# Kernel tuning notes

Measured on AMD Instinct MI355X. Metric: run time of the kernel, lower is better.

## Reference

```python
import jax, jax.numpy as jnp
import numpy as np

B, D, H, W = 2, 16, 16, 16
N = D * H * W
CDESC = 64
TEMP = 0.07
TOPK = 24
RADIUS = 0.45


def flatten_spatial(x):
    # (B, C, D, H, W) -> (B, N, C)
    b, c = x.shape[:2]
    return x.reshape(b, c, -1).transpose(0, 2, 1)


def voxel_grid():
    # normalized voxel-center grid in [-1, 1], shape (3, D, H, W)
    zs = jnp.linspace(-1.0, 1.0, D)
    ys = jnp.linspace(-1.0, 1.0, H)
    xs = jnp.linspace(-1.0, 1.0, W)
    return jnp.stack(jnp.meshgrid(zs, ys, xs, indexing='ij'), axis=0)


def setup_inputs() -> dict:
    key = jax.random.key(0)
    ks = jax.random.split(key, 8)
    return {
        'src_canonical': jax.random.normal(ks[0], (B, 3, D, H, W), jnp.float32),
        'tgt_canonical': jax.random.normal(ks[1], (B, 3, D, H, W), jnp.float32),
        'src_desc': jax.random.normal(ks[2], (B, CDESC, D, H, W), jnp.float32),
        'tgt_desc': jax.random.normal(ks[3], (B, CDESC, D, H, W), jnp.float32),
        'src_mlogits': jax.random.normal(ks[4], (B, 2, D, H, W), jnp.float32),
        'tgt_mlogits': jax.random.normal(ks[5], (B, 2, D, H, W), jnp.float32),
        'src_unc': jax.random.uniform(ks[6], (B, 1, D, H, W), jnp.float32),
        'tgt_unc': jax.random.uniform(ks[7], (B, 1, D, H, W), jnp.float32),
    }


def reference(src_canonical, tgt_canonical, src_desc, tgt_desc,
              src_mlogits, tgt_mlogits, src_unc, tgt_unc):
    sc = flatten_spatial(src_canonical)  # (B, N, 3)
    tc = flatten_spatial(tgt_canonical)  # (B, N, 3)
    sd = flatten_spatial(src_desc)       # (B, N, C)
    td = flatten_spatial(tgt_desc)       # (B, N, C)

    # torch.cdist: Euclidean distance matrix (B, N, N)
    d2 = (jnp.sum(sc * sc, -1)[:, :, None]
          + jnp.sum(tc * tc, -1)[:, None, :]
          - 2.0 * jnp.einsum('bid,bjd->bij', sc, tc))
    dist = jnp.sqrt(jnp.maximum(d2, 1e-12))

    sim = jnp.einsum('bid,bjd->bij', sd, td)  # (B, N, N)

    k = min(TOPK, N)
    _, nn_idx = jax.lax.top_k(-dist, k)  # k smallest distances per row
    bidx = jnp.arange(B)[:, None, None]
    ridx = jnp.arange(N)[None, :, None]
    allowed = jnp.zeros((B, N, N), bool).at[bidx, ridx, nn_idx].set(True)
    allowed = allowed | (dist <= RADIUS)

    tgt_match = jax.nn.softmax(flatten_spatial(tgt_mlogits), axis=-1)[..., 0]  # (B, N)
    src_match = jax.nn.softmax(flatten_spatial(src_mlogits), axis=-1)[..., 0]  # (B, N)

    # (B, N, 1) + (B, 1, N) rank-1 uncertainty penalty
    unc = flatten_spatial(src_unc) + flatten_spatial(tgt_unc).transpose(0, 2, 1)

    scores = sim - dist - 0.1 * unc
    scores = jnp.where(allowed, scores, -10000.0)
    # legacy matchability score mode
    scores = scores + jnp.maximum(jnp.log(tgt_match), -20.0)[:, None, :]
    probs = jax.nn.softmax(scores / TEMP, axis=-1)
    probs = jnp.nan_to_num(probs, nan=0.0, posinf=0.0, neginf=0.0)

    tpos = voxel_grid().reshape(3, -1).T  # (N, 3)
    expected = jnp.einsum('bij,jd->bid', probs, tpos)  # (B, N, 3)
    src_pos = jnp.broadcast_to(tpos, (B, N, 3))

    disp = (expected - src_pos).transpose(0, 2, 1).reshape(B, 3, D, H, W)
    disp = jnp.nan_to_num(disp, nan=0.0, posinf=0.0, neginf=0.0)

    conf = (jnp.max(probs, axis=-1) * src_match).reshape(B, 1, D, H, W)

    ent = -jnp.sum(probs * jnp.log(jnp.clip(probs, 1e-12, None)), axis=-1)
    ent = jnp.nan_to_num(ent, nan=0.0, posinf=0.0, neginf=0.0).reshape(B, 1, D, H, W)

    return expected, disp, probs, conf, ent, src_pos
```

## Files before the change

### kernel.cpp

```cpp
#include <hip/hip_runtime.h>
#include <math.h>
#include <stddef.h>

#define NN    4096
#define BATCH 2
#define CD    64
#define KSEL  24
#define RAD2  0.2025f
#define NBINS 256
#define KBASE 1888
#define LCAP  255
#define CCAP  64

typedef float f4v __attribute__((ext_vector_type(4)));

__device__ __forceinline__ int d2key(unsigned bits) {
  int k = (int)(bits >> 19) - KBASE;
  return k < 0 ? 0 : (k > NBINS - 1 ? NBINS - 1 : k);
}

__device__ __forceinline__ int wave_bin24(const int* h0, const int* h1, int lane, int* cb_out) {
  int4 a = ((const int4*)h0)[lane];
  int4 b = ((const int4*)h1)[lane];
  int tt[4] = {a.x + b.x, a.y + b.y, a.z + b.z, a.w + b.w};
  int s = tt[0] + tt[1] + tt[2] + tt[3];
  int inc = s;
#pragma unroll
  for (int off = 1; off < 64; off <<= 1) {
    int t = __shfl_up(inc, off);
    if (lane >= off) inc += t;
  }
  int below = inc - s;
  int Bl = -1, Bb = 0;
#pragma unroll
  for (int q = 0; q < 4; ++q) {
    if (Bl < 0 && below < KSEL && below + tt[q] >= KSEL) { Bl = 4 * lane + q; Bb = below; }
    below += tt[q];
  }
  unsigned long long mk = __ballot(Bl >= 0);
  if (!mk) return -1;
  int sl = __ffsll((long long)mk) - 1;
  *cb_out = __shfl(Bb, sl);
  return __shfl(Bl, sl);
}

__global__ __launch_bounds__(256)
void prep_all(const float* __restrict__ td, const float* __restrict__ sd,
              const float* __restrict__ tml, const float* __restrict__ tu,
              float* __restrict__ tdT, float* __restrict__ sdT,
              float* __restrict__ addj) {
  __shared__ float tile[64][65];
  int blk = blockIdx.x;
  if (blk < 256) {
    const float* src = (blk < 128) ? td  : sd;
    float*       dst = (blk < 128) ? tdT : sdT;
    int lb = blk & 127;
    int b  = lb >> 6;
    int j0 = (lb & 63) << 6;
    int jl = threadIdx.x & 63;
    int cq = threadIdx.x >> 6;
    const float* srcp = src + (size_t)b * CD * NN;
#pragma unroll
    for (int r = 0; r < 16; ++r) {
      int c = r * 4 + cq;
      tile[c][jl] = srcp[(size_t)c * NN + j0 + jl];
    }
    __syncthreads();
    float* dstp = dst + (size_t)b * NN * CD;
#pragma unroll
    for (int r = 0; r < 16; ++r) {
      int j = r * 4 + cq;
      dstp[(size_t)(j0 + j) * CD + jl] = tile[jl][j];
    }
  } else {
    int idx = (blk - 256) * 256 + threadIdx.x;
    if (idx < BATCH * NN) {
      int b = idx >> 12, j = idx & (NN - 1);
      float l0 = tml[(size_t)b * 2 * NN + j];
      float l1 = tml[(size_t)b * 2 * NN + NN + j];
      float x  = l1 - l0;
      float sp = fmaxf(x, 0.0f) + log1pf(expf(-fabsf(x)));
      addj[idx] = fmaxf(-sp, -20.0f) - 0.1f * tu[idx];
    }
  }
}

__global__ __launch_bounds__(256, 8)
void matcher_main(const float* __restrict__ sc, const float* __restrict__ tc,
                  const float* __restrict__ sd, const float* __restrict__ td,
                  const float* __restrict__ tdT, const float* __restrict__ sdT,
                  const float* __restrict__ addj,
                  const float* __restrict__ tml, const float* __restrict__ tu,
                  const float* __restrict__ sml,
                  float* __restrict__ oexp, float* __restrict__ odisp,
                  float* __restrict__ oprob, float* __restrict__ oconf,
                  float* __restrict__ oent, float* __restrict__ osrc) {
  __shared__ __align__(16) unsigned idxb[NN / 4];
  __shared__ __align__(16) int      hist[2][NBINS];
  __shared__ __align__(16) float4   sdp4[CD / 4];
  __shared__ int2     lst[LCAP];
  __shared__ int2     slist[256];
  __shared__ unsigned cand[CCAP];
  __shared__ int      lcount, candn;

  const int tid  = threadIdx.x;
  const int w    = tid >> 6;
  const int lane = tid & 63;
  const int row  = blockIdx.x;
  const int b    = row >> 12;
  const int i    = row & (NN - 1);
  const unsigned RADB = __float_as_uint(RAD2);

  if (tid < 128) ((int4*)hist)[tid] = make_int4(0, 0, 0, 0);
#pragma unroll
  for (int q = 0; q < 4; ++q) idxb[(q << 8) + tid] = 0u;
  if (sdT) { if (tid < 16) sdp4[tid] = ((const float4*)(sdT + ((size_t)b * NN + i) * CD))[tid]; }
  else     { if (tid < 64) ((float*)sdp4)[tid] = sd[(size_t)b * CD * NN + (size_t)tid * NN + i]; }
  if (tid == 0) { lcount = 0; candn = 0; }

  const float* scb = sc + (size_t)b * 3 * NN;
  const float s0 = scb[i], s1 = scb[NN + i], s2 = scb[2 * NN + i];
  const float4* tcx = (const float4*)(tc + (size_t)b * 3 * NN);
  const float4* tcy = tcx + NN / 4;
  const float4* tcz = tcy + NN / 4;
  const int cp = w >> 1;
  __syncthreads();

  unsigned d2b[16];
#pragma unroll
  for (int k = 0; k < 4; ++k) {
    int g = (k << 8) + tid;
    float4 X = tcx[g], Y = tcy[g], Z = tcz[g];
    float xs[4] = {X.x, X.y, X.z, X.w};
    float ys[4] = {Y.x, Y.y, Y.z, Y.w};
    float zs[4] = {Z.x, Z.y, Z.z, Z.w};
#pragma unroll
    for (int r = 0; r < 4; ++r) {
      float dx = xs[r] - s0, dy = ys[r] - s1, dz = zs[r] - s2;
      float d2 = fmaxf(__fmaf_rn(dx, dx, __fmaf_rn(dy, dy, dz * dz)), 1e-12f);
      unsigned bits = __float_as_uint(d2);
      d2b[(k << 2) + r] = bits;
      if (d2 < 2.0f) atomicAdd(&hist[cp][d2key(bits)], 1);
    }
  }
  __syncthreads();

  int cb = 0;
  int Bs = wave_bin24(hist[0], hist[1], lane, &cb);
  if (Bs < 0) {
    __syncthreads();
#pragma unroll
    for (int m = 0; m < 16; ++m)
      if (__uint_as_float(d2b[m]) >= 2.0f) atomicAdd(&hist[cp][d2key(d2b[m])], 1);
    __syncthreads();
    Bs = wave_bin24(hist[0], hist[1], lane, &cb);
  }

#pragma unroll
  for (int m = 0; m < 16; ++m) {
    unsigned bits = d2b[m];
    int key = d2key(bits);
    if (key <= Bs || bits <= RADB) {
      int idx = atomicAdd(&lcount, 1);
      if (idx < LCAP) {
        int j = ((m >> 2) << 10) + (tid << 2) + (m & 3);
        ((unsigned char*)idxb)[j] = (unsigned char)(idx + 1);
        lst[idx] = make_int2(j, (int)bits);
      }
      if (key == Bs) {
        int c = atomicAdd(&candn, 1);
        if (c < CCAP) cand[c] = bits;
      }
    }
  }
  __syncthreads();
  const int na = lcount < LCAP ? lcount : LCAP;

  unsigned thrb;
  {
    int found = 0; unsigned fv = 0;
    const int Krem = KSEL - cb;
    if (candn <= CCAP) {
      int nc = candn;
      if (lane < nc) {
        unsigned v = cand[lane];
        int lt = 0, le = 0;
        for (int m = 0; m < nc; ++m) { unsigned u = cand[m]; lt += (u < v); le += (u <= v); }
        if (lt < Krem && le >= Krem) { found = 1; fv = v; }
      }
    } else {
      for (int e = lane; e < na; e += 64) {
        unsigned v = (unsigned)lst[e].y;
        int lt = 0, le = 0;
        for (int m = 0; m < na; ++m) {
          unsigned u = (unsigned)lst[m].y;
          lt += (u < v); le += (u <= v);
        }
        if (lt < KSEL && le >= KSEL) { found = 1; fv = v; }
      }
    }
    unsigned long long mk = __ballot(found != 0);
    unsigned d24 = (unsigned)__shfl((int)fv, __ffsll((long long)mk) - 1);
    thrb = d24 > RADB ? d24 : RADB;
  }

  const float* tdb = tdT ? tdT + (size_t)b * NN * CD : nullptr;
  if (tid < na) {
    int2 en = lst[tid];
    int j = en.x;
    unsigned bits = (unsigned)en.y;
    float d2 = __uint_as_float(bits);
    float a0 = 0.f, a1 = 0.f, a2 = 0.f, a3 = 0.f;
    if (tdb) {
      const float4* trow = (const float4*)(tdb + (size_t)j * CD);
#pragma unroll
      for (int q = 0; q < CD / 4; q += 4) {
        float4 x0 = sdp4[q],     t0 = trow[q];
        float4 x1 = sdp4[q + 1], t1 = trow[q + 1];
        float4 x2 = sdp4[q + 2], t2 = trow[q + 2];
        float4 x3 = sdp4[q + 3], t3 = trow[q + 3];
        a0 = fmaf(x0.x, t0.x, fmaf(x0.y, t0.y, fmaf(x0.z, t0.z, fmaf(x0.w, t0.w, a0))));
        a1 = fmaf(x1.x, t1.x, fmaf(x1.y, t1.y, fmaf(x1.z, t1.z, fmaf(x1.w, t1.w, a1))));
        a2 = fmaf(x2.x, t2.x, fmaf(x2.y, t2.y, fmaf(x2.z, t2.z, fmaf(x2.w, t2.w, a2))));
        a3 = fmaf(x3.x, t3.x, fmaf(x3.y, t3.y, fmaf(x3.z, t3.z, fmaf(x3.w, t3.w, a3))));
      }
    } else {
      const float* spx = (const float*)sdp4;
      const float* tp  = td + (size_t)b * CD * NN + j;
#pragma unroll 8
      for (int c2 = 0; c2 < CD; ++c2) a0 = fmaf(spx[c2], tp[(size_t)c2 * NN], a0);
    }
    float sim = (a0 + a1) + (a2 + a3);
    float aj;
    if (addj) {
      aj = addj[(size_t)b * NN + j];
    } else {
      float l0 = tml[(size_t)b * 2 * NN + j];
      float l1 = tml[(size_t)b * 2 * NN + NN + j];
      float x  = l1 - l0;
      float sp = fmaxf(x, 0.0f) + log1pf(expf(-fabsf(x)));
      aj = fmaxf(-sp, -20.0f) - 0.1f * tu[(size_t)b * NN + j];
    }
    float sco = (bits <= thrb) ? (sim - sqrtf(d2) + aj) : -1e30f;
    slist[tid] = make_int2(j, __float_as_int(sco));
  }
  __syncthreads();

  const float C1   = (1.0f / 0.07f) * 1.44269504089f;
  const float STEP = 2.0f / 15.0f;
  const float LN2  = 0.69314718056f;
  float m_ = -1e30f;
  for (int e = lane; e < na; e += 64) m_ = fmaxf(m_, __int_as_float(slist[e].y));
#pragma unroll
  for (int off = 32; off; off >>= 1) m_ = fmaxf(m_, __shfl_xor(m_, off));
  float zl = 0.f, eu = 0.f, e0 = 0.f, e1 = 0.f, e2 = 0.f;
  for (int e = lane; e < na; e += 64) {
    int2 sv = slist[e];
    float u  = (__int_as_float(sv.y) - m_) * C1;
    float ev = exp2f(u);
    int j = sv.x;
    float pz = -1.0f + STEP * (float)(j >> 8);
    float py = -1.0f + STEP * (float)((j >> 4) & 15);
    float px = -1.0f + STEP * (float)(j & 15);
    zl += ev; eu = fmaf(ev, u, eu);
    e0 = fmaf(ev, pz, e0); e1 = fmaf(ev, py, e1); e2 = fmaf(ev, px, e2);
  }
#pragma unroll
  for (int off = 32; off; off >>= 1) {
    zl += __shfl_xor(zl, off); eu += __shfl_xor(eu, off);
    e0 += __shfl_xor(e0, off); e1 += __shfl_xor(e1, off); e2 += __shfl_xor(e2, off);
  }
  const float invZ = 1.0f / zl;

  f4v* prow4 = (f4v*)(oprob + (size_t)row * NN);
#pragma unroll
  for (int q = 0; q < 4; ++q) {
    int c = (q << 8) + tid;
    unsigned pk = idxb[c];
    f4v v; v[0] = 0.f; v[1] = 0.f; v[2] = 0.f; v[3] = 0.f;
    if (pk) {
#pragma unroll
      for (int r = 0; r < 4; ++r) {
        unsigned u8 = (pk >> (8 * r)) & 0xFFu;
        if (u8) v[r] = exp2f((__int_as_float(slist[u8 - 1].y) - m_) * C1) * invZ;
      }
    }
    __builtin_nontemporal_store(v, &prow4[c]);
  }

  if (tid == 0) {
    float p0 = e0 * invZ, p1 = e1 * invZ, p2 = e2 * invZ;
    float ent = LN2 * (log2f(zl) - eu * invZ);
    float tz = -1.0f + STEP * (float)(i >> 8);
    float ty = -1.0f + STEP * (float)((i >> 4) & 15);
    float tx = -1.0f + STEP * (float)(i & 15);
    size_t r3 = (size_t)row * 3;
    oexp[r3 + 0] = p0; oexp[r3 + 1] = p1; oexp[r3 + 2] = p2;
    osrc[r3 + 0] = tz; osrc[r3 + 1] = ty; osrc[r3 + 2] = tx;
    size_t db = (size_t)b * 3 * NN;
    odisp[db + 0 * NN + i] = p0 - tz;
    odisp[db + 1 * NN + i] = p1 - ty;
    odisp[db + 2 * NN + i] = p2 - tx;
    float ls0 = sml[(size_t)b * 2 * NN + i];
    float ls1 = sml[(size_t)b * 2 * NN + NN + i];
    float smv = 1.0f / (1.0f + expf(ls1 - ls0));
    oconf[(size_t)b * NN + i] = invZ * smv;
    oent[(size_t)b * NN + i]  = ent;
  }
}

extern "C" void kernel_launch(void* const* d_in, const int* in_sizes, int n_in,
                              void* d_out, int out_size, void* d_ws, size_t ws_size,
                              hipStream_t stream) {
  const float* sc  = (const float*)d_in[0];
  const float* tc  = (const float*)d_in[1];
  const float* sd  = (const float*)d_in[2];
  const float* td  = (const float*)d_in[3];
  const float* sml = (const float*)d_in[4];
  const float* tml = (const float*)d_in[5];
  const float* tu  = (const float*)d_in[7];

  float* out   = (float*)d_out;
  float* oexp  = out;
  float* odisp = oexp  + (size_t)BATCH * NN * 3;
  float* oprob = odisp + (size_t)BATCH * NN * 3;
  float* oconf = oprob + (size_t)BATCH * NN * NN;
  float* oent  = oconf + (size_t)BATCH * NN;
  float* osrc  = oent  + (size_t)BATCH * NN;

  size_t need = ((size_t)2 * BATCH * NN * CD + (size_t)BATCH * NN) * sizeof(float);
  float* tdT = nullptr; float* sdT = nullptr; float* adj = nullptr;
  if (ws_size >= need) {
    tdT = (float*)d_ws;
    sdT = tdT + (size_t)BATCH * NN * CD;
    adj = sdT + (size_t)BATCH * NN * CD;
    prep_all<<<256 + 32, 256, 0, stream>>>(td, sd, tml, tu, tdT, sdT, adj);
  }
  matcher_main<<<BATCH * NN, 256, 0, stream>>>(sc, tc, sd, td, tdT, sdT, adj,
                                               tml, tu, sml,
                                               oexp, odisp, oprob, oconf, oent, osrc);
}
```

Measured before the change: 194.1 us.

## Process two source rows per 512-thread block sharing target coordinate loads

Each block of 512 threads now handles two adjacent source rows. Every target coordinate load is reused for both rows' distance and histogram computation, and the histogram is split into four copies per row to cut atomic contention. Later stages (threshold search, similarity, softmax, prob row store) are split by thread half. This halves the block count and target-coordinate traffic per row, at the cost of more shared memory per block and a heavier launch-bounds target that could lower occupancy or spill registers.

```diff
diff --git a/kernel.cpp b/kernel.cpp
--- a/kernel.cpp
+++ b/kernel.cpp
@@ -11,6 +11,7 @@
 #define KBASE 1888
 #define LCAP  255
 #define CCAP  64
+#define NCP   4
 
 typedef float f4v __attribute__((ext_vector_type(4)));
 
@@ -19,10 +20,13 @@
   return k < 0 ? 0 : (k > NBINS - 1 ? NBINS - 1 : k);
 }
 
-__device__ __forceinline__ int wave_bin24(const int* h0, const int* h1, int lane, int* cb_out) {
-  int4 a = ((const int4*)h0)[lane];
-  int4 b = ((const int4*)h1)[lane];
-  int tt[4] = {a.x + b.x, a.y + b.y, a.z + b.z, a.w + b.w};
+__device__ __forceinline__ int wave_bin24(const int (*h)[NBINS], int lane, int* cb_out) {
+  int4 a = ((const int4*)h[0])[lane];
+  int4 b = ((const int4*)h[1])[lane];
+  int4 c = ((const int4*)h[2])[lane];
+  int4 d = ((const int4*)h[3])[lane];
+  int tt[4] = {a.x + b.x + c.x + d.x, a.y + b.y + c.y + d.y,
+               a.z + b.z + c.z + d.z, a.w + b.w + c.w + d.w};
   int s = tt[0] + tt[1] + tt[2] + tt[3];
   int inc = s;
 #pragma unroll
@@ -85,7 +89,7 @@
   }
 }
 
-__global__ __launch_bounds__(256, 8)
+__global__ __launch_bounds__(512, 8)
 void matcher_main(const float* __restrict__ sc, const float* __restrict__ tc,
                   const float* __restrict__ sd, const float* __restrict__ td,
                   const float* __restrict__ tdT, const float* __restrict__ sdT,
@@ -95,105 +99,133 @@
                   float* __restrict__ oexp, float* __restrict__ odisp,
                   float* __restrict__ oprob, float* __restrict__ oconf,
                   float* __restrict__ oent, float* __restrict__ osrc) {
-  __shared__ __align__(16) unsigned idxb[NN / 4];
-  __shared__ __align__(16) int      hist[2][NBINS];
-  __shared__ __align__(16) float4   sdp4[CD / 4];
-  __shared__ int2     lst[LCAP];
-  __shared__ int2     slist[256];
-  __shared__ unsigned cand[CCAP];
-  __shared__ int      lcount, candn;
+  __shared__ __align__(16) unsigned idxb[2][NN / 4];
+  __shared__ __align__(16) int      hist[2][NCP][NBINS];
+  __shared__ __align__(16) float4   sdp4[2][CD / 4];
+  __shared__ int2     lst[2][LCAP];
+  __shared__ int2     slist[2][256];
+  __shared__ unsigned cand[2][CCAP];
+  __shared__ int      lcount[2], candn[2];
 
   const int tid  = threadIdx.x;
   const int w    = tid >> 6;
   const int lane = tid & 63;
-  const int row  = blockIdx.x;
-  const int b    = row >> 12;
-  const int i    = row & (NN - 1);
+  const int rg   = tid >> 8;
+  const int row0 = blockIdx.x * 2;
+  const int b    = row0 >> 12;
+  const int i0   = row0 & (NN - 1);
   const unsigned RADB = __float_as_uint(RAD2);
 
-  if (tid < 128) ((int4*)hist)[tid] = make_int4(0, 0, 0, 0);
-#pragma unroll
-  for (int q = 0; q < 4; ++q) idxb[(q << 8) + tid] = 0u;
-  if (sdT) { if (tid < 16) sdp4[tid] = ((const float4*)(sdT + ((size_t)b * NN + i) * CD))[tid]; }
-  else     { if (tid < 64) ((float*)sdp4)[tid] = sd[(size_t)b * CD * NN + (size_t)tid * NN + i]; }
-  if (tid == 0) { lcount = 0; candn = 0; }
-
+  ((int4*)hist)[tid] = make_int4(0, 0, 0, 0);
+  ((int4*)idxb)[tid] = make_int4(0, 0, 0, 0);
+  if (tid < 2) { lcount[tid] = 0; candn[tid] = 0; }
+  if (sdT) {
+    if (tid < 32) {
+      int r = tid >> 4, t = tid & 15;
+      sdp4[r][t] = ((const float4*)(sdT + ((size_t)b * NN + i0 + r) * CD))[t];
+    }
+  } else if (tid < 128) {
+    int r = tid >> 6, c = tid & 63;
+    ((float*)sdp4[r])[c] = sd[(size_t)b * CD * NN + (size_t)c * NN + i0 + r];
+  }
   const float* scb = sc + (size_t)b * 3 * NN;
-  const float s0 = scb[i], s1 = scb[NN + i], s2 = scb[2 * NN + i];
+  const float sA0 = scb[i0],     sA1 = scb[NN + i0],     sA2 = scb[2 * NN + i0];
+  const float sB0 = scb[i0 + 1], sB1 = scb[NN + i0 + 1], sB2 = scb[2 * NN + i0 + 1];
   const float4* tcx = (const float4*)(tc + (size_t)b * 3 * NN);
   const float4* tcy = tcx + NN / 4;
   const float4* tcz = tcy + NN / 4;
-  const int cp = w >> 1;
+  const int cp = w & (NCP - 1);
   __syncthreads();
 
-  unsigned d2b[16];
-#pragma unroll
-  for (int k = 0; k < 4; ++k) {
-    int g = (k << 8) + tid;
+  unsigned dA[8], dB[8];
+#pragma unroll
+  for (int k = 0; k < 2; ++k) {
+    int g = (k << 9) + tid;
     float4 X = tcx[g], Y = tcy[g], Z = tcz[g];
     float xs[4] = {X.x, X.y, X.z, X.w};
     float ys[4] = {Y.x, Y.y, Y.z, Y.w};
     float zs[4] = {Z.x, Z.y, Z.z, Z.w};
 #pragma unroll
     for (int r = 0; r < 4; ++r) {
-      float dx = xs[r] - s0, dy = ys[r] - s1, dz = zs[r] - s2;
+      float dx = xs[r] - sA0, dy = ys[r] - sA1, dz = zs[r] - sA2;
       float d2 = fmaxf(__fmaf_rn(dx, dx, __fmaf_rn(dy, dy, dz * dz)), 1e-12f);
       unsigned bits = __float_as_uint(d2);
-      d2b[(k << 2) + r] = bits;
-      if (d2 < 2.0f) atomicAdd(&hist[cp][d2key(bits)], 1);
+      dA[(k << 2) + r] = bits;
+      if (d2 < 2.0f) atomicAdd(&hist[0][cp][d2key(bits)], 1);
+      dx = xs[r] - sB0; dy = ys[r] - sB1; dz = zs[r] - sB2;
+      d2 = fmaxf(__fmaf_rn(dx, dx, __fmaf_rn(dy, dy, dz * dz)), 1e-12f);
+      bits = __float_as_uint(d2);
+      dB[(k << 2) + r] = bits;
+      if (d2 < 2.0f) atomicAdd(&hist[1][cp][d2key(bits)], 1);
     }
   }
   __syncthreads();
 
-  int cb = 0;
-  int Bs = wave_bin24(hist[0], hist[1], lane, &cb);
-  if (Bs < 0) {
+  int cbA = 0, cbB = 0;
+  int BsA = wave_bin24(hist[0], lane, &cbA);
+  int BsB = wave_bin24(hist[1], lane, &cbB);
+  if (BsA < 0 || BsB < 0) {
     __syncthreads();
-#pragma unroll
-    for (int m = 0; m < 16; ++m)
-      if (__uint_as_float(d2b[m]) >= 2.0f) atomicAdd(&hist[cp][d2key(d2b[m])], 1);
+    if (BsA < 0) {
+#pragma unroll
+      for (int m = 0; m < 8; ++m)
+        if (__uint_as_float(dA[m]) >= 2.0f) atomicAdd(&hist[0][cp][d2key(dA[m])], 1);
+    }
+    if (BsB < 0) {
+#pragma unroll
+      for (int m = 0; m < 8; ++m)
+        if (__uint_as_float(dB[m]) >= 2.0f) atomicAdd(&hist[1][cp][d2key(dB[m])], 1);
+    }
     __syncthreads();
-    Bs = wave_bin24(hist[0], hist[1], lane, &cb);
-  }
-
-#pragma unroll
-  for (int m = 0; m < 16; ++m) {
-    unsigned bits = d2b[m];
+    if (BsA < 0) BsA = wave_bin24(hist[0], lane, &cbA);
+    if (BsB < 0) BsB = wave_bin24(hist[1], lane, &cbB);
+  }
+
+#pragma unroll
+  for (int m = 0; m < 8; ++m) {
+    int j = ((m >> 2) << 11) + (tid << 2) + (m & 3);
+    unsigned bits = dA[m];
     int key = d2key(bits);
-    if (key <= Bs || bits <= RADB) {
-      int idx = atomicAdd(&lcount, 1);
+    if (key <= BsA || bits <= RADB) {
+      int idx = atomicAdd(&lcount[0], 1);
       if (idx < LCAP) {
-        int j = ((m >> 2) << 10) + (tid << 2) + (m & 3);
-        ((unsigned char*)idxb)[j] = (unsigned char)(idx + 1);
-        lst[idx] = make_int2(j, (int)bits);
-      }
-      if (key == Bs) {
-        int c = atomicAdd(&candn, 1);
-        if (c < CCAP) cand[c] = bits;
-      }
+        ((unsigned char*)idxb[0])[j] = (unsigned char)(idx + 1);
+        lst[0][idx] = make_int2(j, (int)bits);
+      }
+      if (key == BsA) { int cc = atomicAdd(&candn[0], 1); if (cc < CCAP) cand[0][cc] = bits; }
+    }
+    bits = dB[m];
+    key = d2key(bits);
+    if (key <= BsB || bits <= RADB) {
+      int idx = atomicAdd(&lcount[1], 1);
+      if (idx < LCAP) {
+        ((unsigned char*)idxb[1])[j] = (unsigned char)(idx + 1);
+        lst[1][idx] = make_int2(j, (int)bits);
+      }
+      if (key == BsB) { int cc = atomicAdd(&candn[1], 1); if (cc < CCAP) cand[1][cc] = bits; }
     }
   }
   __syncthreads();
-  const int na = lcount < LCAP ? lcount : LCAP;
+  const int nag = (lcount[rg] < LCAP) ? lcount[rg] : LCAP;
 
   unsigned thrb;
   {
     int found = 0; unsigned fv = 0;
-    const int Krem = KSEL - cb;
-    if (candn <= CCAP) {
-      int nc = candn;
-      if (lane < nc) {
-        unsigned v = cand[lane];
+    const int Krem = KSEL - (rg ? cbB : cbA);
+    const int ncg  = candn[rg];
+    if (ncg <= CCAP) {
+      if (lane < ncg) {
+        unsigned v = cand[rg][lane];
         int lt = 0, le = 0;
-        for (int m = 0; m < nc; ++m) { unsigned u = cand[m]; lt += (u < v); le += (u <= v); }
+        for (int m = 0; m < ncg; ++m) { unsigned u = cand[rg][m]; lt += (u < v); le += (u <= v); }
         if (lt < Krem && le >= Krem) { found = 1; fv = v; }
       }
     } else {
-      for (int e = lane; e < na; e += 64) {
-        unsigned v = (unsigned)lst[e].y;
+      for (int e = lane; e < nag; e += 64) {
+        unsigned v = (unsigned)lst[rg][e].y;
         int lt = 0, le = 0;
-        for (int m = 0; m < na; ++m) {
-          unsigned u = (unsigned)lst[m].y;
+        for (int m = 0; m < nag; ++m) {
+          unsigned u = (unsigned)lst[rg][m].y;
           lt += (u < v); le += (u <= v);
         }
         if (lt < KSEL && le >= KSEL) { found = 1; fv = v; }
@@ -205,27 +237,29 @@
   }
 
   const float* tdb = tdT ? tdT + (size_t)b * NN * CD : nullptr;
-  if (tid < na) {
-    int2 en = lst[tid];
+  const int e5 = tid & 255;
+  if (e5 < nag) {
+    int2 en = lst[rg][e5];
     int j = en.x;
     unsigned bits = (unsigned)en.y;
     float d2 = __uint_as_float(bits);
+    const float4* sp4 = (const float4*)sdp4[rg];
     float a0 = 0.f, a1 = 0.f, a2 = 0.f, a3 = 0.f;
     if (tdb) {
       const float4* trow = (const float4*)(tdb + (size_t)j * CD);
 #pragma unroll
       for (int q = 0; q < CD / 4; q += 4) {
-        float4 x0 = sdp4[q],     t0 = trow[q];
-        float4 x1 = sdp4[q + 1], t1 = trow[q + 1];
-        float4 x2 = sdp4[q + 2], t2 = trow[q + 2];
-        float4 x3 = sdp4[q + 3], t3 = trow[q + 3];
+        float4 x0 = sp4[q],     t0 = trow[q];
+        float4 x1 = sp4[q + 1], t1 = trow[q + 1];
+        float4 x2 = sp4[q + 2], t2 = trow[q + 2];
+        float4 x3 = sp4[q + 3], t3 = trow[q + 3];
         a0 = fmaf(x0.x, t0.x, fmaf(x0.y, t0.y, fmaf(x0.z, t0.z, fmaf(x0.w, t0.w, a0))));
         a1 = fmaf(x1.x, t1.x, fmaf(x1.y, t1.y, fmaf(x1.z, t1.z, fmaf(x1.w, t1.w, a1))));
         a2 = fmaf(x2.x, t2.x, fmaf(x2.y, t2.y, fmaf(x2.z, t2.z, fmaf(x2.w, t2.w, a2))));
         a3 = fmaf(x3.x, t3.x, fmaf(x3.y, t3.y, fmaf(x3.z, t3.z, fmaf(x3.w, t3.w, a3))));
       }
     } else {
-      const float* spx = (const float*)sdp4;
+      const float* spx = (const float*)sdp4[rg];
       const float* tp  = td + (size_t)b * CD * NN + j;
 #pragma unroll 8
       for (int c2 = 0; c2 < CD; ++c2) a0 = fmaf(spx[c2], tp[(size_t)c2 * NN], a0);
@@ -242,7 +276,7 @@
       aj = fmaxf(-sp, -20.0f) - 0.1f * tu[(size_t)b * NN + j];
     }
     float sco = (bits <= thrb) ? (sim - sqrtf(d2) + aj) : -1e30f;
-    slist[tid] = make_int2(j, __float_as_int(sco));
+    slist[rg][e5] = make_int2(j, __float_as_int(sco));
   }
   __syncthreads();
 
@@ -250,12 +284,12 @@
   const float STEP = 2.0f / 15.0f;
   const float LN2  = 0.69314718056f;
   float m_ = -1e30f;
-  for (int e = lane; e < na; e += 64) m_ = fmaxf(m_, __int_as_float(slist[e].y));
+  for (int e = lane; e < nag; e += 64) m_ = fmaxf(m_, __int_as_float(slist[rg][e].y));
 #pragma unroll
   for (int off = 32; off; off >>= 1) m_ = fmaxf(m_, __shfl_xor(m_, off));
   float zl = 0.f, eu = 0.f, e0 = 0.f, e1 = 0.f, e2 = 0.f;
-  for (int e = lane; e < na; e += 64) {
-    int2 sv = slist[e];
+  for (int e = lane; e < nag; e += 64) {
+    int2 sv = slist[rg][e];
     float u  = (__int_as_float(sv.y) - m_) * C1;
     float ev = exp2f(u);
     int j = sv.x;
@@ -272,40 +306,42 @@
   }
   const float invZ = 1.0f / zl;
 
-  f4v* prow4 = (f4v*)(oprob + (size_t)row * NN);
+  const int wl = w & 3;
+  f4v* prow4 = (f4v*)(oprob + (size_t)(row0 + rg) * NN);
 #pragma unroll
   for (int q = 0; q < 4; ++q) {
-    int c = (q << 8) + tid;
-    unsigned pk = idxb[c];
+    int c = (q << 8) + (wl << 6) + lane;
+    unsigned pk = idxb[rg][c];
     f4v v; v[0] = 0.f; v[1] = 0.f; v[2] = 0.f; v[3] = 0.f;
     if (pk) {
 #pragma unroll
       for (int r = 0; r < 4; ++r) {
         unsigned u8 = (pk >> (8 * r)) & 0xFFu;
-        if (u8) v[r] = exp2f((__int_as_float(slist[u8 - 1].y) - m_) * C1) * invZ;
+        if (u8) v[r] = exp2f((__int_as_float(slist[rg][u8 - 1].y) - m_) * C1) * invZ;
       }
     }
     __builtin_nontemporal_store(v, &prow4[c]);
   }
 
-  if (tid == 0) {
+  if ((tid & 255) == 0) {
+    int i_ = i0 + rg, row = row0 + rg;
     float p0 = e0 * invZ, p1 = e1 * invZ, p2 = e2 * invZ;
     float ent = LN2 * (log2f(zl) - eu * invZ);
-    float tz = -1.0f + STEP * (float)(i >> 8);
-    float ty = -1.0f + STEP * (float)((i >> 4) & 15);
-    float tx = -1.0f + STEP * (float)(i & 15);
+    float tz = -1.0f + STEP * (float)(i_ >> 8);
+    float ty = -1.0f + STEP * (float)((i_ >> 4) & 15);
+    float tx = -1.0f + STEP * (float)(i_ & 15);
     size_t r3 = (size_t)row * 3;
     oexp[r3 + 0] = p0; oexp[r3 + 1] = p1; oexp[r3 + 2] = p2;
     osrc[r3 + 0] = tz; osrc[r3 + 1] = ty; osrc[r3 + 2] = tx;
     size_t db = (size_t)b * 3 * NN;
-    odisp[db + 0 * NN + i] = p0 - tz;
-    odisp[db + 1 * NN + i] = p1 - ty;
-    odisp[db + 2 * NN + i] = p2 - tx;
-    float ls0 = sml[(size_t)b * 2 * NN + i];
-    float ls1 = sml[(size_t)b * 2 * NN + NN + i];
+    odisp[db + 0 * NN + i_] = p0 - tz;
+    odisp[db + 1 * NN + i_] = p1 - ty;
+    odisp[db + 2 * NN + i_] = p2 - tx;
+    float ls0 = sml[(size_t)b * 2 * NN + i_];
+    float ls1 = sml[(size_t)b * 2 * NN + NN + i_];
     float smv = 1.0f / (1.0f + expf(ls1 - ls0));
-    oconf[(size_t)b * NN + i] = invZ * smv;
-    oent[(size_t)b * NN + i]  = ent;
+    oconf[(size_t)b * NN + i_] = invZ * smv;
+    oent[(size_t)b * NN + i_]  = ent;
   }
 }
 
@@ -336,7 +372,7 @@
     adj = sdT + (size_t)BATCH * NN * CD;
     prep_all<<<256 + 32, 256, 0, stream>>>(td, sd, tml, tu, tdT, sdT, adj);
   }
-  matcher_main<<<BATCH * NN, 256, 0, stream>>>(sc, tc, sd, td, tdT, sdT, adj,
-                                               tml, tu, sml,
-                                               oexp, odisp, oprob, oconf, oent, osrc);
-}
+  matcher_main<<<BATCH * NN / 2, 512, 0, stream>>>(sc, tc, sd, td, tdT, sdT, adj,
+                                                   tml, tu, sml,
+                                                   oexp, odisp, oprob, oconf, oent, osrc);
+}
```

Result: slower. 201.4 us (+3.8%).
